# Optimization experiments

Measured on AMD Instinct MI355X. Metric: run time of the kernel, lower is better.

Reference implementation:

```python
import jax, jax.numpy as jnp
import numpy as np

N_NODES = 50000
N_EDGES = 800000
D = 128            # in_channels == hidden_channels
N_LAYERS = 3
OUT = 16
N_GRAPHS = 128


def setup_inputs() -> dict:
    key = jax.random.key(0)
    ks = jax.random.split(key, 12)
    x = jax.random.normal(ks[0], (N_NODES, D), dtype=jnp.float32)
    edge_index = jax.random.randint(ks[1], (2, N_EDGES), 0, N_NODES, dtype=jnp.int64)
    batch_ids = jnp.sort(jax.random.randint(ks[2], (N_NODES,), 0, N_GRAPHS, dtype=jnp.int64))
    s = 1.0 / np.sqrt(D)
    # Stacked per-layer GraphConv weights (all layers are D->D here).
    Wrel = jax.random.uniform(ks[3], (N_LAYERS, D, D), jnp.float32, -s, s)
    brel = jax.random.uniform(ks[4], (N_LAYERS, D), jnp.float32, -s, s)
    Wroot = jax.random.uniform(ks[5], (N_LAYERS, D, D), jnp.float32, -s, s)
    # post_mp MLP head
    W1 = jax.random.uniform(ks[6], (D, D), jnp.float32, -s, s)
    b1 = jax.random.uniform(ks[7], (D,), jnp.float32, -s, s)
    W2 = jax.random.uniform(ks[8], (D, OUT), jnp.float32, -s, s)
    b2 = jax.random.uniform(ks[9], (OUT,), jnp.float32, -s, s)
    return {"x": x, "edge_index": edge_index, "batch_ids": batch_ids,
            "Wrel": Wrel, "brel": brel, "Wroot": Wroot,
            "W1": W1, "b1": b1, "W2": W2, "b2": b2}


def reference(x, edge_index, batch_ids, Wrel, brel, Wroot, W1, b1, W2, b2):
    src, dst = edge_index[0], edge_index[1]
    h = x
    for l in range(N_LAYERS):
        # GraphConv: lin_rel(sum_{j->i} h_j) + lin_root(h_i)
        agg = jax.ops.segment_sum(h[src], dst, num_segments=N_NODES)  # [N, D]
        h = agg @ Wrel[l] + brel[l] + h @ Wroot[l]
        h = jax.nn.relu(h)
        # dropout p=0.0 / eval mode -> identity
    # global mean pool over graphs
    sums = jax.ops.segment_sum(h, batch_ids, num_segments=N_GRAPHS)          # [G, D]
    counts = jax.ops.segment_sum(jnp.ones((N_NODES,), h.dtype), batch_ids,
                                 num_segments=N_GRAPHS)                       # [G]
    pooled = sums / jnp.maximum(counts, 1.0)[:, None]
    # post_mp MLP (dropout identity in eval)
    out = (pooled @ W1 + b1) @ W2 + b2                                        # [G, OUT]
    return out
```

## Files before the change

### kernel.cpp

```cpp
#include <hip/hip_runtime.h>

#define N_NODES 50000
#define N_EDGES 800000
#define D 128
#define N_LAYERS 3
#define OUT_F 16
#define N_GRAPHS 128
#define NBUCK 391
#define EPB 4096
#define NB3 ((N_EDGES + EPB - 1) / EPB)
#define CAP 4096
#define NT32 ((N_NODES + 31) / 32)
#define PITCH 132

typedef __attribute__((ext_vector_type(8))) short short8;
typedef __attribute__((ext_vector_type(16))) float floatx16;

__device__ __forceinline__ unsigned short f2bf(float f) {
  unsigned int u = __float_as_uint(f);
  u += 0x7fff + ((u >> 16) & 1);
  return (unsigned short)(u >> 16);
}
__device__ __forceinline__ float bf2f(unsigned short b) {
  return __uint_as_float(((unsigned int)b) << 16);
}
__device__ __forceinline__ float blo(unsigned v) { return __uint_as_float(v << 16); }
__device__ __forceinline__ float bhi(unsigned v) { return __uint_as_float(v & 0xffff0000u); }

__global__ __launch_bounds__(256) void partition_kernel(
    const int* __restrict__ src, const int* __restrict__ dst,
    int* __restrict__ cursor, unsigned* __restrict__ pairs) {
  __shared__ unsigned pk[EPB];
  __shared__ int hist[NBUCK];
  __shared__ int wcur[NBUCK];
  const int e0 = blockIdx.x * EPB;
  const int n = min(EPB, N_EDGES - e0);
  const int t = threadIdx.x;
  for (int i = t; i < NBUCK; i += 256) hist[i] = 0;
  __syncthreads();
  for (int i = t; i < n; i += 256) {
    int d = dst[e0 + i], s = src[e0 + i];
    pk[i] = ((unsigned)d << 16) | (unsigned)s;
    atomicAdd(&hist[d >> 7], 1);
  }
  __syncthreads();
  for (int i = t; i < NBUCK; i += 256)
    wcur[i] = i * CAP + (hist[i] ? atomicAdd(&cursor[i], hist[i]) : 0);
  __syncthreads();
  for (int i = t; i < n; i += 256) {
    unsigned p = pk[i];
    int pos = atomicAdd(&wcur[p >> 23], 1);
    pairs[pos] = p;
  }
}

__global__ __launch_bounds__(256) void bucket_sort_kernel(
    const unsigned* __restrict__ pairs, const int* __restrict__ cursor,
    int* __restrict__ rowbeg, int* __restrict__ rowend, int* __restrict__ esrc) {
  __shared__ unsigned pk[CAP];
  __shared__ int sorted[CAP];
  __shared__ int hist[128], off[128], cur[128];
  const int bkt = blockIdx.x;
  const int t = threadIdx.x;
  const int beg = bkt * CAP;
  const int cnt = cursor[bkt];
  if (t < 128) hist[t] = 0;
  __syncthreads();
  for (int i = t; i < cnt; i += 256) {
    unsigned p = pairs[beg + i];
    pk[i] = p;
    atomicAdd(&hist[(p >> 16) & 127], 1);
  }
  __syncthreads();
  if (t < 128) off[t] = hist[t];
  __syncthreads();
  for (int o = 1; o < 128; o <<= 1) {
    int x = (t < 128 && t >= o) ? off[t - o] : 0;
    __syncthreads();
    if (t < 128) off[t] += x;
    __syncthreads();
  }
  if (t < 128) {
    int node = bkt * 128 + t;
    if (node < N_NODES) {
      rowbeg[node] = beg + off[t] - hist[t];
      rowend[node] = beg + off[t];
    }
    cur[t] = off[t] - hist[t];
  }
  __syncthreads();
  for (int i = t; i < cnt; i += 256) {
    unsigned p = pk[i];
    int pos = atomicAdd(&cur[(p >> 16) & 127], 1);
    sorted[pos] = (int)(p & 0xFFFFu);
  }
  __syncthreads();
  for (int i = t; i < cnt; i += 256) esrc[beg + i] = sorted[i];
}

__global__ __launch_bounds__(256) void cast_x_kernel(
    const float* __restrict__ x, unsigned short* __restrict__ x16) {
  int i = blockIdx.x * 256 + threadIdx.x;
  if ((size_t)i * 4 >= (size_t)N_NODES * D) return;
  const float4 v = *(const float4*)&x[(size_t)i * 4];
  uint2 o;
  o.x = f2bf(v.x) | ((unsigned)f2bf(v.y) << 16);
  o.y = f2bf(v.z) | ((unsigned)f2bf(v.w) << 16);
  *(uint2*)&x16[(size_t)i * 4] = o;
}

__global__ __launch_bounds__(256) void prep_w_kernel(
    const float* __restrict__ Wrel, const float* __restrict__ Wroot,
    unsigned short* __restrict__ wt) {
  int idx = blockIdx.x * 256 + threadIdx.x;
  if (idx >= N_LAYERS * 2 * 2 * 32 * 64) return;
  const int lane = idx & 63;
  const int kst = (idx >> 6) & 31;
  const int nt = (idx >> 11) & 1;
  const int half = (idx >> 12) & 1;
  const int l = idx >> 13;
  const int n = half * 64 + nt * 32 + (lane & 31);
  const int kx0 = kst * 16 + (lane >> 5) * 8;
  const int seg = kx0 >> 7;
  const int k0 = kx0 & 127;
  const int mat = seg >> 1, lo = seg & 1;
  const float* W = (mat ? Wroot : Wrel) + (size_t)l * D * D;
  unsigned short v[8];
#pragma unroll
  for (int j = 0; j < 8; ++j) {
    float w = W[(size_t)(k0 + j) * D + n];
    unsigned short hi = f2bf(w);
    v[j] = lo ? f2bf(w - bf2f(hi)) : hi;
  }
  unsigned short* dstp =
      wt + ((size_t)l * 128 + (half * 2 + nt) * 32 + kst) * 512 + lane * 8;
  *(uint4*)dstp = *(const uint4*)v;
}

__global__ __launch_bounds__(256, 2) void layer_kernel(
    const unsigned short* __restrict__ h,
    const int* __restrict__ rowbeg, const int* __restrict__ rowend,
    const int* __restrict__ esrc,
    const unsigned short* __restrict__ wt,
    const float* __restrict__ brel,
    unsigned short* __restrict__ outp) {
  __shared__ unsigned short atile[32 * PITCH];
  __shared__ unsigned short htile[32 * PITCH];
  const int t = threadIdx.x;
  const int r0 = blockIdx.x * 32;
  const int g = t >> 4, li = t & 15;
  const unsigned short* hp = h + (size_t)li * 8;

#pragma unroll
  for (int rr = 0; rr < 2; ++rr) {
    const int lr = rr * 16 + g;
    const int row = r0 + lr;
    if (row < N_NODES)
      *(uint4*)&htile[lr * PITCH + li * 8] =
          *(const uint4*)&h[(size_t)row * D + li * 8];
  }

#pragma unroll
  for (int rr = 0; rr < 2; ++rr) {
    const int lr = rr * 16 + g;
    const int row = r0 + lr;
    int beg = 0, end = 0;
    if (row < N_NODES) { beg = rowbeg[row]; end = rowend[row]; }
    float a0 = 0, a1 = 0, a2 = 0, a3 = 0, a4 = 0, a5 = 0, a6 = 0, a7 = 0;
    int e = beg;
    for (; e + 4 <= end; e += 4) {
      const int s0 = esrc[e],     s1 = esrc[e + 1];
      const int s2 = esrc[e + 2], s3 = esrc[e + 3];
      const uint4 v0 = *(const uint4*)&hp[(size_t)s0 * D];
      const uint4 v1 = *(const uint4*)&hp[(size_t)s1 * D];
      const uint4 v2 = *(const uint4*)&hp[(size_t)s2 * D];
      const uint4 v3 = *(const uint4*)&hp[(size_t)s3 * D];
      a0 += blo(v0.x) + blo(v1.x) + blo(v2.x) + blo(v3.x);
      a1 += bhi(v0.x) + bhi(v1.x) + bhi(v2.x) + bhi(v3.x);
      a2 += blo(v0.y) + blo(v1.y) + blo(v2.y) + blo(v3.y);
      a3 += bhi(v0.y) + bhi(v1.y) + bhi(v2.y) + bhi(v3.y);
      a4 += blo(v0.z) + blo(v1.z) + blo(v2.z) + blo(v3.z);
      a5 += bhi(v0.z) + bhi(v1.z) + bhi(v2.z) + bhi(v3.z);
      a6 += blo(v0.w) + blo(v1.w) + blo(v2.w) + blo(v3.w);
      a7 += bhi(v0.w) + bhi(v1.w) + bhi(v2.w) + bhi(v3.w);
    }
    for (; e < end; ++e) {
      const uint4 v0 = *(const uint4*)&hp[(size_t)esrc[e] * D];
      a0 += blo(v0.x); a1 += bhi(v0.x);
      a2 += blo(v0.y); a3 += bhi(v0.y);
      a4 += blo(v0.z); a5 += bhi(v0.z);
      a6 += blo(v0.w); a7 += bhi(v0.w);
    }
    uint4 o;
    o.x = f2bf(a0) | ((unsigned)f2bf(a1) << 16);
    o.y = f2bf(a2) | ((unsigned)f2bf(a3) << 16);
    o.z = f2bf(a4) | ((unsigned)f2bf(a5) << 16);
    o.w = f2bf(a6) | ((unsigned)f2bf(a7) << 16);
    *(uint4*)&atile[lr * PITCH + li * 8] = o;
  }
  __syncthreads();

  const int wave = t >> 6, lane = t & 63;
  const int r2 = lane & 31, hseg = lane >> 5;
  short8 ag[8], hh[8];
#pragma unroll
  for (int i = 0; i < 8; ++i) {
    ag[i] = *(const short8*)&atile[r2 * PITCH + i * 16 + hseg * 8];
    hh[i] = *(const short8*)&htile[r2 * PITCH + i * 16 + hseg * 8];
  }
  const unsigned short* ws = wt + (size_t)wave * 32 * 512;
  floatx16 accA = {0.f}, accB = {0.f};
#pragma unroll
  for (int k = 0; k < 16; ++k) {
    const short8 b0 = *(const short8*)&ws[(size_t)k * 512 + lane * 8];
    const short8 b1 = *(const short8*)&ws[(size_t)(16 + k) * 512 + lane * 8];
    accA = __builtin_amdgcn_mfma_f32_32x32x16_bf16(ag[k & 7], b0, accA, 0, 0, 0);
    accB = __builtin_amdgcn_mfma_f32_32x32x16_bf16(hh[k & 7], b1, accB, 0, 0, 0);
  }
  const int cb = wave * 32 + r2;
  const float bias = brel[cb];
#pragma unroll
  for (int reg = 0; reg < 16; ++reg) {
    const int row = r0 + (reg & 3) + 8 * (reg >> 2) + 4 * hseg;
    if (row < N_NODES)
      outp[(size_t)row * D + cb] =
          f2bf(fmaxf(accA[reg] + accB[reg] + bias, 0.f));
  }
}

__device__ __forceinline__ int lb_search(const int* __restrict__ a, int n, int key) {
  int lo = 0, hi = n;
  while (lo < hi) {
    int m = (lo + hi) >> 1;
    if (a[m] < key) lo = m + 1; else hi = m;
  }
  return lo;
}

__global__ __launch_bounds__(256) void pool_head_kernel(
    const unsigned short* __restrict__ h, const int* __restrict__ batch,
    const float* __restrict__ W1, const float* __restrict__ b1,
    const float* __restrict__ W2, const float* __restrict__ b2,
    float* __restrict__ out) {
  __shared__ float sums_lds[16][128];
  __shared__ float pooled[128];
  __shared__ float hidden[128];
  __shared__ int range[2];
  const int g = blockIdx.x;
  const int t = threadIdx.x;
  if (t < 2) range[t] = lb_search(batch, N_NODES, g + t);
  __syncthreads();
  const int lo = range[0], hi = range[1];
  const int rg = t >> 4, cg = t & 15;
  float a0 = 0, a1 = 0, a2 = 0, a3 = 0, a4 = 0, a5 = 0, a6 = 0, a7 = 0;
  for (int n = lo + rg; n < hi; n += 16) {
    const uint4 v = *(const uint4*)&h[(size_t)n * D + cg * 8];
    a0 += blo(v.x); a1 += bhi(v.x);
    a2 += blo(v.y); a3 += bhi(v.y);
    a4 += blo(v.z); a5 += bhi(v.z);
    a6 += blo(v.w); a7 += bhi(v.w);
  }
  sums_lds[rg][cg * 8 + 0] = a0; sums_lds[rg][cg * 8 + 1] = a1;
  sums_lds[rg][cg * 8 + 2] = a2; sums_lds[rg][cg * 8 + 3] = a3;
  sums_lds[rg][cg * 8 + 4] = a4; sums_lds[rg][cg * 8 + 5] = a5;
  sums_lds[rg][cg * 8 + 6] = a6; sums_lds[rg][cg * 8 + 7] = a7;
  __syncthreads();
  if (t < 128) {
    float s = 0.f;
#pragma unroll
    for (int r = 0; r < 16; ++r) s += sums_lds[r][t];
    pooled[t] = s / fmaxf((float)(hi - lo), 1.f);
  }
  __syncthreads();
  if (t < 128) {
    float a = b1[t];
    for (int k = 0; k < D; ++k) a += pooled[k] * W1[k * D + t];
    hidden[t] = a;
  }
  __syncthreads();
  if (t < OUT_F) {
    float o = b2[t];
    for (int k = 0; k < D; ++k) o += hidden[k] * W2[k * OUT_F + t];
    out[(size_t)g * OUT_F + t] = o;
  }
}

extern "C" void kernel_launch(void* const* d_in, const int* in_sizes, int n_in,
                              void* d_out, int out_size, void* d_ws, size_t ws_size,
                              hipStream_t stream) {
  const float* x     = (const float*)d_in[0];
  const int*   ei    = (const int*)d_in[1];
  const int*   batch = (const int*)d_in[2];
  const float* Wrel  = (const float*)d_in[3];
  const float* brel  = (const float*)d_in[4];
  const float* Wroot = (const float*)d_in[5];
  const float* W1    = (const float*)d_in[6];
  const float* b1    = (const float*)d_in[7];
  const float* W2    = (const float*)d_in[8];
  const float* b2    = (const float*)d_in[9];
  float* out = (float*)d_out;

  const size_t ND = (size_t)N_NODES * D;
  unsigned short* bufA = (unsigned short*)d_ws;
  unsigned short* bufB = bufA + ND;
  unsigned short* bufC = bufB + ND;
  unsigned short* wt   = bufC + ND;
  int* rowbeg = (int*)(wt + (size_t)N_LAYERS * 128 * 512);
  int* rowend = rowbeg + N_NODES;
  int* esrc   = rowend + N_NODES;
  unsigned* pairs = (unsigned*)(esrc + (size_t)NBUCK * CAP);
  int* cursor = (int*)(pairs + (size_t)NBUCK * CAP);

  const int* esrc_in = ei;
  const int* edst_in = ei + N_EDGES;

  hipMemsetAsync(cursor, 0, NBUCK * sizeof(int), stream);
  partition_kernel<<<NB3, 256, 0, stream>>>(esrc_in, edst_in, cursor, pairs);
  bucket_sort_kernel<<<NBUCK, 256, 0, stream>>>(pairs, cursor, rowbeg, rowend, esrc);

  cast_x_kernel<<<(int)((ND / 4 + 255) / 256), 256, 0, stream>>>(x, bufC);
  prep_w_kernel<<<(N_LAYERS * 2 * 2 * 32 * 64 + 255) / 256, 256, 0, stream>>>(
      Wrel, Wroot, wt);

  const size_t WL = (size_t)128 * 512;
  layer_kernel<<<NT32, 256, 0, stream>>>(bufC, rowbeg, rowend, esrc,
                                         wt, brel, bufA);
  layer_kernel<<<NT32, 256, 0, stream>>>(bufA, rowbeg, rowend, esrc,
                                         wt + WL, brel + D, bufB);
  layer_kernel<<<NT32, 256, 0, stream>>>(bufB, rowbeg, rowend, esrc,
                                         wt + 2 * WL, brel + 2 * D, bufA);

  pool_head_kernel<<<N_GRAPHS, 256, 0, stream>>>(bufA, batch, W1, b1, W2, b2, out);
}
```

Baseline: 267.4 us.

## Double layer-kernel threads per row tile and merge prep kernels into one launch

Result: no change. 264.1 us (-1.2%).

```diff
diff --git a/kernel.cpp b/kernel.cpp
--- a/kernel.cpp
+++ b/kernel.cpp
@@ -12,6 +12,8 @@
 #define CAP 4096
 #define NT32 ((N_NODES + 31) / 32)
 #define PITCH 132
+#define NCAST 6250
+#define NPREPW 96
 
 typedef __attribute__((ext_vector_type(8))) short short8;
 typedef __attribute__((ext_vector_type(16))) float floatx16;
@@ -98,46 +100,49 @@
   for (int i = t; i < cnt; i += 256) esrc[beg + i] = sorted[i];
 }
 
-__global__ __launch_bounds__(256) void cast_x_kernel(
-    const float* __restrict__ x, unsigned short* __restrict__ x16) {
-  int i = blockIdx.x * 256 + threadIdx.x;
-  if ((size_t)i * 4 >= (size_t)N_NODES * D) return;
-  const float4 v = *(const float4*)&x[(size_t)i * 4];
-  uint2 o;
-  o.x = f2bf(v.x) | ((unsigned)f2bf(v.y) << 16);
-  o.y = f2bf(v.z) | ((unsigned)f2bf(v.w) << 16);
-  *(uint2*)&x16[(size_t)i * 4] = o;
-}
-
-__global__ __launch_bounds__(256) void prep_w_kernel(
+__global__ __launch_bounds__(256) void prep_all_kernel(
+    const float* __restrict__ x, unsigned short* __restrict__ x16,
     const float* __restrict__ Wrel, const float* __restrict__ Wroot,
-    unsigned short* __restrict__ wt) {
-  int idx = blockIdx.x * 256 + threadIdx.x;
-  if (idx >= N_LAYERS * 2 * 2 * 32 * 64) return;
-  const int lane = idx & 63;
-  const int kst = (idx >> 6) & 31;
-  const int nt = (idx >> 11) & 1;
-  const int half = (idx >> 12) & 1;
-  const int l = idx >> 13;
-  const int n = half * 64 + nt * 32 + (lane & 31);
-  const int kx0 = kst * 16 + (lane >> 5) * 8;
-  const int seg = kx0 >> 7;
-  const int k0 = kx0 & 127;
-  const int mat = seg >> 1, lo = seg & 1;
-  const float* W = (mat ? Wroot : Wrel) + (size_t)l * D * D;
-  unsigned short v[8];
-#pragma unroll
-  for (int j = 0; j < 8; ++j) {
-    float w = W[(size_t)(k0 + j) * D + n];
-    unsigned short hi = f2bf(w);
-    v[j] = lo ? f2bf(w - bf2f(hi)) : hi;
-  }
-  unsigned short* dstp =
-      wt + ((size_t)l * 128 + (half * 2 + nt) * 32 + kst) * 512 + lane * 8;
-  *(uint4*)dstp = *(const uint4*)v;
-}
-
-__global__ __launch_bounds__(256, 2) void layer_kernel(
+    unsigned short* __restrict__ wt, int* __restrict__ cursor) {
+  const int bid = blockIdx.x;
+  const int t = threadIdx.x;
+  if (bid < NCAST) {
+    const int i = bid * 256 + t;
+    const float4 v = *(const float4*)&x[(size_t)i * 4];
+    uint2 o;
+    o.x = f2bf(v.x) | ((unsigned)f2bf(v.y) << 16);
+    o.y = f2bf(v.z) | ((unsigned)f2bf(v.w) << 16);
+    *(uint2*)&x16[(size_t)i * 4] = o;
+  } else if (bid < NCAST + NPREPW) {
+    const int idx = (bid - NCAST) * 256 + t;
+    const int lane = idx & 63;
+    const int kst = (idx >> 6) & 31;
+    const int nt = (idx >> 11) & 1;
+    const int half = (idx >> 12) & 1;
+    const int l = idx >> 13;
+    const int n = half * 64 + nt * 32 + (lane & 31);
+    const int kx0 = kst * 16 + (lane >> 5) * 8;
+    const int seg = kx0 >> 7;
+    const int k0 = kx0 & 127;
+    const int mat = seg >> 1, lo = seg & 1;
+    const float* W = (mat ? Wroot : Wrel) + (size_t)l * D * D;
+    unsigned short v[8];
+#pragma unroll
+    for (int j = 0; j < 8; ++j) {
+      float w = W[(size_t)(k0 + j) * D + n];
+      unsigned short hi = f2bf(w);
+      v[j] = lo ? f2bf(w - bf2f(hi)) : hi;
+    }
+    unsigned short* dstp =
+        wt + ((size_t)l * 128 + (half * 2 + nt) * 32 + kst) * 512 + lane * 8;
+    *(uint4*)dstp = *(const uint4*)v;
+  } else {
+    const int i = (bid - NCAST - NPREPW) * 256 + t;
+    if (i < NBUCK) cursor[i] = 0;
+  }
+}
+
+__global__ __launch_bounds__(512, 8) void layer_kernel(
     const unsigned short* __restrict__ h,
     const int* __restrict__ rowbeg, const int* __restrict__ rowend,
     const int* __restrict__ esrc,
@@ -146,85 +151,88 @@
     unsigned short* __restrict__ outp) {
   __shared__ unsigned short atile[32 * PITCH];
   __shared__ unsigned short htile[32 * PITCH];
+  __shared__ float redB[4][16][64];
   const int t = threadIdx.x;
   const int r0 = blockIdx.x * 32;
   const int g = t >> 4, li = t & 15;
+  const int row = r0 + g;
   const unsigned short* hp = h + (size_t)li * 8;
 
-#pragma unroll
-  for (int rr = 0; rr < 2; ++rr) {
-    const int lr = rr * 16 + g;
-    const int row = r0 + lr;
-    if (row < N_NODES)
-      *(uint4*)&htile[lr * PITCH + li * 8] =
-          *(const uint4*)&h[(size_t)row * D + li * 8];
-  }
-
-#pragma unroll
-  for (int rr = 0; rr < 2; ++rr) {
-    const int lr = rr * 16 + g;
-    const int row = r0 + lr;
-    int beg = 0, end = 0;
-    if (row < N_NODES) { beg = rowbeg[row]; end = rowend[row]; }
-    float a0 = 0, a1 = 0, a2 = 0, a3 = 0, a4 = 0, a5 = 0, a6 = 0, a7 = 0;
-    int e = beg;
-    for (; e + 4 <= end; e += 4) {
-      const int s0 = esrc[e],     s1 = esrc[e + 1];
-      const int s2 = esrc[e + 2], s3 = esrc[e + 3];
-      const uint4 v0 = *(const uint4*)&hp[(size_t)s0 * D];
-      const uint4 v1 = *(const uint4*)&hp[(size_t)s1 * D];
-      const uint4 v2 = *(const uint4*)&hp[(size_t)s2 * D];
-      const uint4 v3 = *(const uint4*)&hp[(size_t)s3 * D];
-      a0 += blo(v0.x) + blo(v1.x) + blo(v2.x) + blo(v3.x);
-      a1 += bhi(v0.x) + bhi(v1.x) + bhi(v2.x) + bhi(v3.x);
-      a2 += blo(v0.y) + blo(v1.y) + blo(v2.y) + blo(v3.y);
-      a3 += bhi(v0.y) + bhi(v1.y) + bhi(v2.y) + bhi(v3.y);
-      a4 += blo(v0.z) + blo(v1.z) + blo(v2.z) + blo(v3.z);
-      a5 += bhi(v0.z) + bhi(v1.z) + bhi(v2.z) + bhi(v3.z);
-      a6 += blo(v0.w) + blo(v1.w) + blo(v2.w) + blo(v3.w);
-      a7 += bhi(v0.w) + bhi(v1.w) + bhi(v2.w) + bhi(v3.w);
-    }
-    for (; e < end; ++e) {
-      const uint4 v0 = *(const uint4*)&hp[(size_t)esrc[e] * D];
-      a0 += blo(v0.x); a1 += bhi(v0.x);
-      a2 += blo(v0.y); a3 += bhi(v0.y);
-      a4 += blo(v0.z); a5 += bhi(v0.z);
-      a6 += blo(v0.w); a7 += bhi(v0.w);
-    }
+  if (row < N_NODES) {
+    *(uint4*)&htile[g * PITCH + li * 8] =
+        *(const uint4*)&h[(size_t)row * D + li * 8];
+  } else {
+    const uint4 z = {0, 0, 0, 0};
+    *(uint4*)&htile[g * PITCH + li * 8] = z;
+  }
+
+  int beg = 0, end = 0;
+  if (row < N_NODES) { beg = rowbeg[row]; end = rowend[row]; }
+  float a0 = 0, a1 = 0, a2 = 0, a3 = 0, a4 = 0, a5 = 0, a6 = 0, a7 = 0;
+  int e = beg;
+  for (; e + 4 <= end; e += 4) {
+    const int s0 = esrc[e],     s1 = esrc[e + 1];
+    const int s2 = esrc[e + 2], s3 = esrc[e + 3];
+    const uint4 v0 = *(const uint4*)&hp[(size_t)s0 * D];
+    const uint4 v1 = *(const uint4*)&hp[(size_t)s1 * D];
+    const uint4 v2 = *(const uint4*)&hp[(size_t)s2 * D];
+    const uint4 v3 = *(const uint4*)&hp[(size_t)s3 * D];
+    a0 += blo(v0.x) + blo(v1.x) + blo(v2.x) + blo(v3.x);
+    a1 += bhi(v0.x) + bhi(v1.x) + bhi(v2.x) + bhi(v3.x);
+    a2 += blo(v0.y) + blo(v1.y) + blo(v2.y) + blo(v3.y);
+    a3 += bhi(v0.y) + bhi(v1.y) + bhi(v2.y) + bhi(v3.y);
+    a4 += blo(v0.z) + blo(v1.z) + blo(v2.z) + blo(v3.z);
+    a5 += bhi(v0.z) + bhi(v1.z) + bhi(v2.z) + bhi(v3.z);
+    a6 += blo(v0.w) + blo(v1.w) + blo(v2.w) + blo(v3.w);
+    a7 += bhi(v0.w) + bhi(v1.w) + bhi(v2.w) + bhi(v3.w);
+  }
+  for (; e < end; ++e) {
+    const uint4 v0 = *(const uint4*)&hp[(size_t)esrc[e] * D];
+    a0 += blo(v0.x); a1 += bhi(v0.x);
+    a2 += blo(v0.y); a3 += bhi(v0.y);
+    a4 += blo(v0.z); a5 += bhi(v0.z);
+    a6 += blo(v0.w); a7 += bhi(v0.w);
+  }
+  {
     uint4 o;
     o.x = f2bf(a0) | ((unsigned)f2bf(a1) << 16);
     o.y = f2bf(a2) | ((unsigned)f2bf(a3) << 16);
     o.z = f2bf(a4) | ((unsigned)f2bf(a5) << 16);
     o.w = f2bf(a6) | ((unsigned)f2bf(a7) << 16);
-    *(uint4*)&atile[lr * PITCH + li * 8] = o;
+    *(uint4*)&atile[g * PITCH + li * 8] = o;
   }
   __syncthreads();
 
   const int wave = t >> 6, lane = t & 63;
+  const int p = wave & 3, chain = wave >> 2;
   const int r2 = lane & 31, hseg = lane >> 5;
-  short8 ag[8], hh[8];
-#pragma unroll
-  for (int i = 0; i < 8; ++i) {
-    ag[i] = *(const short8*)&atile[r2 * PITCH + i * 16 + hseg * 8];
-    hh[i] = *(const short8*)&htile[r2 * PITCH + i * 16 + hseg * 8];
-  }
-  const unsigned short* ws = wt + (size_t)wave * 32 * 512;
-  floatx16 accA = {0.f}, accB = {0.f};
+  const unsigned short* tile = chain ? htile : atile;
+  short8 fr[8];
+#pragma unroll
+  for (int i = 0; i < 8; ++i)
+    fr[i] = *(const short8*)&tile[r2 * PITCH + i * 16 + hseg * 8];
+  const unsigned short* ws = wt + (size_t)(p * 32 + chain * 16) * 512;
+  floatx16 acc = {0.f};
 #pragma unroll
   for (int k = 0; k < 16; ++k) {
-    const short8 b0 = *(const short8*)&ws[(size_t)k * 512 + lane * 8];
-    const short8 b1 = *(const short8*)&ws[(size_t)(16 + k) * 512 + lane * 8];
-    accA = __builtin_amdgcn_mfma_f32_32x32x16_bf16(ag[k & 7], b0, accA, 0, 0, 0);
-    accB = __builtin_amdgcn_mfma_f32_32x32x16_bf16(hh[k & 7], b1, accB, 0, 0, 0);
-  }
-  const int cb = wave * 32 + r2;
-  const float bias = brel[cb];
-#pragma unroll
-  for (int reg = 0; reg < 16; ++reg) {
-    const int row = r0 + (reg & 3) + 8 * (reg >> 2) + 4 * hseg;
-    if (row < N_NODES)
-      outp[(size_t)row * D + cb] =
-          f2bf(fmaxf(accA[reg] + accB[reg] + bias, 0.f));
+    const short8 b = *(const short8*)&ws[(size_t)k * 512 + lane * 8];
+    acc = __builtin_amdgcn_mfma_f32_32x32x16_bf16(fr[k & 7], b, acc, 0, 0, 0);
+  }
+  if (chain) {
+#pragma unroll
+    for (int reg = 0; reg < 16; ++reg) redB[p][reg][lane] = acc[reg];
+  }
+  __syncthreads();
+  if (!chain) {
+    const int cb = p * 32 + r2;
+    const float bias = brel[cb];
+#pragma unroll
+    for (int reg = 0; reg < 16; ++reg) {
+      const int orow = r0 + (reg & 3) + 8 * (reg >> 2) + 4 * hseg;
+      if (orow < N_NODES)
+        outp[(size_t)orow * D + cb] =
+            f2bf(fmaxf(acc[reg] + redB[p][reg][lane] + bias, 0.f));
+    }
   }
 }
 
@@ -314,20 +322,17 @@
   const int* esrc_in = ei;
   const int* edst_in = ei + N_EDGES;
 
-  hipMemsetAsync(cursor, 0, NBUCK * sizeof(int), stream);
+  prep_all_kernel<<<NCAST + NPREPW + 2, 256, 0, stream>>>(
+      x, bufC, Wrel, Wroot, wt, cursor);
   partition_kernel<<<NB3, 256, 0, stream>>>(esrc_in, edst_in, cursor, pairs);
   bucket_sort_kernel<<<NBUCK, 256, 0, stream>>>(pairs, cursor, rowbeg, rowend, esrc);
 
-  cast_x_kernel<<<(int)((ND / 4 + 255) / 256), 256, 0, stream>>>(x, bufC);
-  prep_w_kernel<<<(N_LAYERS * 2 * 2 * 32 * 64 + 255) / 256, 256, 0, stream>>>(
-      Wrel, Wroot, wt);
-
   const size_t WL = (size_t)128 * 512;
-  layer_kernel<<<NT32, 256, 0, stream>>>(bufC, rowbeg, rowend, esrc,
+  layer_kernel<<<NT32, 512, 0, stream>>>(bufC, rowbeg, rowend, esrc,
                                          wt, brel, bufA);
-  layer_kernel<<<NT32, 256, 0, stream>>>(bufA, rowbeg, rowend, esrc,
+  layer_kernel<<<NT32, 512, 0, stream>>>(bufA, rowbeg, rowend, esrc,
                                          wt + WL, brel + D, bufB);
-  layer_kernel<<<NT32, 256, 0, stream>>>(bufB, rowbeg, rowend, esrc,
+  layer_kernel<<<NT32, 512, 0, stream>>>(bufB, rowbeg, rowend, esrc,
                                          wt + 2 * WL, brel + 2 * D, bufA);
 
   pool_head_kernel<<<N_GRAPHS, 256, 0, stream>>>(bufA, batch, W1, b1, W2, b2, out);
```
